# Performance work log

Hardware: AMD Instinct MI355X
Metric: run time of the kernel (lower is better)

## Reference

```python
import jax, jax.numpy as jnp
import numpy as np

EPS = 1e-5

def _ln(z, g, b):
    # LayerNorm over last axis (per the gammas/betas of shape (2, 3H))
    mu = jnp.mean(z, axis=-1, keepdims=True)
    var = jnp.var(z, axis=-1, keepdims=True)
    return g * (z - mu) * jax.lax.rsqrt(var + EPS) + b

def setup_inputs() -> dict:
    key = jax.random.key(0)
    ks = jax.random.split(key, 12)
    B, L, D_IN, H, A, DEPTH = 64, 512, 256, 256, 128, 4
    glorot = lambda k, sh: jax.random.normal(k, sh, jnp.float32) * np.sqrt(2.0 / (sh[0] + sh[1])).astype(np.float32)
    # variable-length prefix masks (bucketing/masking semantics of the layer)
    lengths = jax.random.randint(ks[0], (B, 1), L // 2, L + 1)
    mask = jnp.arange(L)[None, :] < lengths
    return {
        'x': jax.random.normal(ks[1], (B, L, D_IN), jnp.float32),
        'mask': mask,
        'W_emb': glorot(ks[2], (D_IN, H)),
        'b_emb': jnp.zeros((H,), jnp.float32),
        'W': glorot(ks[3], (H, 3 * H)),
        'U': glorot(ks[4], (H, 3 * H)),
        'b': jnp.zeros((3 * H,), jnp.float32),
        'W_action_1': glorot(ks[5], (H, A)),
        'U_action_1': glorot(ks[6], (H, A)),
        'b_action_1': jnp.zeros((A,), jnp.float32),
        'W_action_2': glorot(ks[7], (A, 2)),
        'b_action_2': jnp.zeros((2,), jnp.float32),
        'gammas': jnp.ones((2, 3 * H), jnp.float32),
        'betas': jnp.zeros((2, 3 * H), jnp.float32),
        'depth': DEPTH,
    }

def _run_depth(x_seq, m_seq, W, U, b, Wa1, Ua1, ba1, Wa2, ba2, gammas, betas):
    # x_seq: (L,B,H), m_seq: (L,B) bool
    H = W.shape[0]
    B = x_seq.shape[1]
    # precompute + layernorm the input projection for all steps (fusable)
    xp_all = _ln(jnp.einsum('lbh,hk->lbk', x_seq, W), gammas[0], betas[0])  # (L,B,3H)

    def step(h, inputs):
        xp, xt, mt = inputs  # (B,3H), (B,H), (B,)
        hp = _ln(h @ U, gammas[1], betas[1])
        r = jax.nn.sigmoid(xp[:, :H] + hp[:, :H] + b[:H])
        z = jax.nn.sigmoid(xp[:, H:2 * H] + hp[:, H:2 * H] + b[H:2 * H])
        hh = jnp.tanh(xp[:, 2 * H:] + r * hp[:, 2 * H:] + b[2 * H:])
        h_new = z * h + (1.0 - z) * hh
        # action-policy subnetwork (binary merge/propagate decision)
        logits = jnp.tanh(xt @ Wa1 + h @ Ua1 + ba1) @ Wa2 + ba2  # (B,2)
        pol = jax.nn.softmax(logits, axis=-1)
        act = (pol[:, 1] > pol[:, 0]) & mt
        h_out = jnp.where(mt[:, None], h_new, h)  # masked steps carry state
        return h_out, (h_out, act, pol)

    h0 = jnp.zeros((B, H), x_seq.dtype)
    _, (h_seq, act_seq, pol_seq) = jax.lax.scan(step, h0, (xp_all, x_seq, m_seq))
    return h_seq, act_seq, pol_seq

def reference(x, mask, W_emb, b_emb, W, U, b, W_action_1, U_action_1, b_action_1,
              W_action_2, b_action_2, gammas, betas, depth):
    # embedding projection, then time-major like the Theano scans
    h_seq = jnp.swapaxes(x @ W_emb + b_emb, 0, 1)  # (L,B,H)
    m_seq = jnp.swapaxes(mask, 0, 1)               # (L,B)
    actions, policies = [], []
    for _ in range(depth):  # vertical (tree-depth) scan: small fixed count
        h_new, act, pol = _run_depth(h_seq, m_seq, W, U, b,
                                     W_action_1, U_action_1, b_action_1,
                                     W_action_2, b_action_2, gammas, betas)
        actions.append(act)
        policies.append(pol)
        h_seq = h_new
        m_seq = m_seq & act  # tree collapse: only selected nodes survive upward
    output = h_seq[-1]  # (B,H) final hidden state of top layer
    action = jnp.stack(actions, 0).transpose(2, 0, 1)      # (B,depth,L)
    policy = jnp.stack(policies, 0).transpose(2, 0, 1, 3)  # (B,depth,L,2)
    return output, action, policy
```

## Files before the change

### kernel.cpp

```cpp
#include <hip/hip_runtime.h>
#include <hip/hip_bf16.h>
#include <math.h>

#define BB 64
#define LL 512
#define HH 256
#define H3 768
#define AA 128
#define NDEPTH 4
#define NROWS (LL*BB)

#define EXCH_U64_PER_CHAIN (2 * 3 * 256)

typedef float vf32x32 __attribute__((ext_vector_type(32)));

__global__ void maskcvt_kernel(const unsigned char* __restrict__ raw,
                               int* __restrict__ m)
{
    int i = blockIdx.x * blockDim.x + threadIdx.x;
    bool bytemode = (raw[1] == 1);
    int v;
    if (bytemode) v = raw[i] ? 1 : 0;
    else          v = (((const int*)raw)[i] != 0) ? 1 : 0;
    m[i] = v;
}

__global__ __launch_bounds__(512) void mkidx_kernel(
    const int* __restrict__ m,
    int* __restrict__ rowidx,
    int* __restrict__ nact)
{
    const int b    = blockIdx.x;
    const int tid  = threadIdx.x;
    const int lane = tid & 63;
    const int w    = tid >> 6;
    __shared__ int wcnt[8];
    int pred = m[b * LL + tid];
    unsigned long long bal = __ballot(pred != 0);
    int below = __popcll(bal & ((1ull << lane) - 1ull));
    if (lane == 63) wcnt[w] = __popcll(bal);
    __syncthreads();
    int woff = 0;
#pragma unroll
    for (int i = 0; i < 8; ++i) woff += (i < w) ? wcnt[i] : 0;
    if (pred) rowidx[b * LL + woff + below] = tid;
    if (tid == 511) nact[b] = woff + wcnt[7];
}

template<int MODE, int EPI>
__global__ __launch_bounds__(256) void gemm_kernel(
    const float* __restrict__ A, const float* __restrict__ Bm,
    const float* __restrict__ bias,
    float* __restrict__ C, int M, int N,
    const int* __restrict__ ridx, const int* __restrict__ nact)
{
    __shared__ float As[16][136];
    __shared__ float Bs[16][136];
    const int tid = threadIdx.x;
    const int tx = tid & 15, ty = tid >> 4;
    const int row0 = blockIdx.y * 128, col0 = blockIdx.x * 128;

    int arow0 = 0, arow1 = 0;
    if (MODE == 3) {
        const int bb = row0 >> 9;
        const int na = nact[bb];
        if ((row0 & 511) >= na) return;
        const int r0 = row0 + (tid >> 2);
        const int r1 = r0 + 64;
        const int l0 = ((r0 & 511) < na) ? ridx[r0] : 0;
        const int l1 = ((r1 & 511) < na) ? ridx[r1] : 0;
        arow0 = l0 * 64 + bb;
        arow1 = l1 * 64 + bb;
    }

    float acc[8][8];
#pragma unroll
    for (int i = 0; i < 8; ++i)
#pragma unroll
        for (int j = 0; j < 8; ++j) acc[i][j] = 0.f;

    for (int kk = 0; kk < 256; kk += 16) {
#pragma unroll
        for (int i = 0; i < 2; ++i) {
            int aid = i * 256 + tid;
            int r   = aid >> 2;
            int k4  = (aid & 3) << 2;
            int rr  = row0 + r;
            float4 v;
            if (MODE == 1) {
                v = *(const float4*)(A + (rr & 63) * 131072 + (rr >> 6) * 256 + kk + k4);
            } else {
                int ar = i ? arow1 : arow0;
                v = *(const float4*)(A + ar * 256 + kk + k4);
            }
            As[k4 + 0][r] = v.x; As[k4 + 1][r] = v.y;
            As[k4 + 2][r] = v.z; As[k4 + 3][r] = v.w;

            int bid = i * 256 + tid;
            int bk  = bid >> 5;
            int c4  = (bid & 31) << 2;
            float4 w = *(const float4*)(Bm + (kk + bk) * N + col0 + c4);
            *(float4*)&Bs[bk][c4] = w;
        }
        __syncthreads();
#pragma unroll
        for (int k = 0; k < 16; ++k) {
            float a[8], bb2[8];
            *(float4*)&a[0]   = *(const float4*)&As[k][ty * 8];
            *(float4*)&a[4]   = *(const float4*)&As[k][ty * 8 + 4];
            *(float4*)&bb2[0] = *(const float4*)&Bs[k][tx * 8];
            *(float4*)&bb2[4] = *(const float4*)&Bs[k][tx * 8 + 4];
#pragma unroll
            for (int i = 0; i < 8; ++i)
#pragma unroll
                for (int j = 0; j < 8; ++j)
                    acc[i][j] += a[i] * bb2[j];
        }
        __syncthreads();
    }

#pragma unroll
    for (int i = 0; i < 8; ++i) {
        int row  = row0 + ty * 8 + i;
        int colb = col0 + tx * 8;
        float vout[8];
#pragma unroll
        for (int j = 0; j < 8; ++j) {
            float v = acc[i][j];
            if (EPI == 1) v += bias[colb + j];
            vout[j] = v;
        }
        *(float4*)&C[row * N + colb]     = *(float4*)&vout[0];
        *(float4*)&C[row * N + colb + 4] = *(float4*)&vout[4];
    }
}

__global__ __launch_bounds__(256) void lnrows_kernel(
    float* __restrict__ XP, const float* __restrict__ g0,
    const float* __restrict__ b0, const float* __restrict__ gb,
    const int* __restrict__ nact)
{
    const int row = blockIdx.x;
    if ((row & 511) >= nact[row >> 9]) return;
    const int tid = threadIdx.x;
    float* p = XP + (long)row * H3;
    float v0 = p[tid], v1 = p[tid + 256], v2 = p[tid + 512];
    float s = v0 + v1 + v2;
    float q = v0 * v0 + v1 * v1 + v2 * v2;
#pragma unroll
    for (int off = 32; off >= 1; off >>= 1) {
        s += __shfl_xor(s, off);
        q += __shfl_xor(q, off);
    }
    __shared__ float rs4[4], rq4[4];
    if ((tid & 63) == 0) { rs4[tid >> 6] = s; rq4[tid >> 6] = q; }
    __syncthreads();
    float S = rs4[0] + rs4[1] + rs4[2] + rs4[3];
    float Q = rq4[0] + rq4[1] + rq4[2] + rq4[3];
    float mu  = S * (1.f / 768.f);
    float var = Q * (1.f / 768.f) - mu * mu;
    float r   = rsqrtf(var + 1e-5f);
    p[tid]       = g0[tid]       * (v0 - mu) * r + b0[tid]       + gb[tid];
    p[tid + 256] = g0[tid + 256] * (v1 - mu) * r + b0[tid + 256] + gb[tid + 256];
    p[tid + 512] = g0[tid + 512] * (v2 - mu) * r + b0[tid + 512] + gb[tid + 512];
}

__global__ __launch_bounds__(512, 2) void scan3_kernel(
    const float* __restrict__ XP,
    const float* __restrict__ U,
    const float* __restrict__ g1, const float* __restrict__ b1,
    const int* __restrict__ mask,
    float* __restrict__ Y,
    unsigned long long* __restrict__ exch,
    int seq0,
    const float* __restrict__ Xc,
    const float* __restrict__ Wa1,
    const float* __restrict__ ba1,
    float* __restrict__ XA)
{
    __shared__ float h_cur[256];
    __shared__ float part[16][256];
    __shared__ float xp_lds[768];
    __shared__ float g1s[768], b1s[768];
    __shared__ int   mk[512];
    __shared__ float reds[4], redq[4];
    __shared__ float As[16][136];
    __shared__ float Bs[16][136];

    const int tid = threadIdx.x;

    if (blockIdx.x >= 192) {
        const int t    = blockIdx.x - 192;
        const int row0 = t * 128;
        const int tx   = tid & 15;
        const int ty4  = tid >> 4;
        float xacc[4][8];
#pragma unroll
        for (int i = 0; i < 4; ++i)
#pragma unroll
            for (int j = 0; j < 8; ++j) xacc[i][j] = 0.f;

        for (int kk = 0; kk < 256; kk += 16) {
            {
                int r  = tid >> 2;
                int k4 = (tid & 3) << 2;
                float4 v = *(const float4*)(Xc + (row0 + r) * 256 + kk + k4);
                As[k4 + 0][r] = v.x; As[k4 + 1][r] = v.y;
                As[k4 + 2][r] = v.z; As[k4 + 3][r] = v.w;
            }
            {
                int bk = tid >> 5;
                int c4 = (tid & 31) << 2;
                float4 w = *(const float4*)(Wa1 + (kk + bk) * AA + c4);
                *(float4*)&Bs[bk][c4] = w;
            }
            __syncthreads();
#pragma unroll
            for (int k = 0; k < 16; ++k) {
                float a[4], bb2[8];
                *(float4*)&a[0]   = *(const float4*)&As[k][ty4 * 4];
                *(float4*)&bb2[0] = *(const float4*)&Bs[k][tx * 8];
                *(float4*)&bb2[4] = *(const float4*)&Bs[k][tx * 8 + 4];
#pragma unroll
                for (int i = 0; i < 4; ++i)
#pragma unroll
                    for (int j = 0; j < 8; ++j)
                        xacc[i][j] += a[i] * bb2[j];
            }
            __syncthreads();
        }
#pragma unroll
        for (int i = 0; i < 4; ++i) {
            int row  = row0 + ty4 * 4 + i;
            int colb = tx * 8;
            float vout[8];
#pragma unroll
            for (int j = 0; j < 8; ++j) vout[j] = xacc[i][j] + ba1[colb + j];
            *(float4*)&XA[row * AA + colb]     = *(float4*)&vout[0];
            *(float4*)&XA[row * AA + colb + 4] = *(float4*)&vout[4];
        }
        return;
    }

    const int i0   = blockIdx.x;
    const int xcd  = i0 & 7;
    const int slot = i0 >> 3;
    const int b    = xcd + 8 * (slot / 3);
    const int s    = slot % 3;
    const int kg   = tid >> 5;
    const int cg   = tid & 31;
    const int q1   = (s + 1 >= 3) ? s - 2 : s + 1;
    const int q2   = (s + 2 >= 3) ? s - 1 : s + 2;

    vf32x32 u0v, u1v, u2v, u3v;
    {
        const volatile float* Uv = U;
        const int colbase = s * 256 + cg;
#pragma unroll
        for (int i = 0; i < 16; ++i) {
#pragma unroll
            for (int j = 0; j < 8; ++j) {
                const int f = i * 8 + j;
                float val = Uv[(kg * 16 + i) * H3 + colbase + 32 * j];
                if      (f < 32) u0v[f]      = val;
                else if (f < 64) u1v[f - 32] = val;
                else if (f < 96) u2v[f - 64] = val;
                else             u3v[f - 96] = val;
            }
        }
    }
    if (tid < 256) h_cur[tid] = 0.f;
    for (int i = tid; i < 768; i += 512) { g1s[i] = g1[i]; b1s[i] = b1[i]; }
    mk[tid] = mask[b * LL + tid];
    __syncthreads();

    unsigned long long* exb = exch + b * EXCH_U64_PER_CHAIN;
    int seq = seq0;

    for (int l = 0; l < LL; ++l) {
        if (!mk[l]) {
            if (s == 0 && tid < 64) {
                float4 hv = *(const float4*)&h_cur[tid * 4];
                *(float4*)&Y[((long)l * BB + b) * HH + tid * 4] = hv;
            }
            continue;
        }
        seq++;
        const int par = seq & 1;
        const int cs  = seq - seq0 - 1;

        float4 xr4;
        if (tid < 192) xr4 = *(const float4*)(XP + ((long)(b * LL + cs)) * H3 + tid * 4);

        float acc[8] = {0.f, 0.f, 0.f, 0.f, 0.f, 0.f, 0.f, 0.f};
#pragma unroll
        for (int i = 0; i < 4; ++i) {
            float4 hv = *(const float4*)&h_cur[kg * 16 + i * 4];
#pragma unroll
            for (int e = 0; e < 4; ++e) {
                const float hh = (e == 0) ? hv.x : (e == 1) ? hv.y
                               : (e == 2) ? hv.z : hv.w;
                const int ik = i * 4 + e;
#pragma unroll
                for (int j = 0; j < 8; ++j) {
                    const int f = ik * 8 + j;
                    const float uu = (f < 32) ? u0v[f]
                                   : (f < 64) ? u1v[f - 32]
                                   : (f < 96) ? u2v[f - 64]
                                   :            u3v[f - 96];
                    acc[j] += uu * hh;
                }
            }
        }
#pragma unroll
        for (int j = 0; j < 8; ++j)
            part[kg][cg + 32 * j] = acc[j];
        __syncthreads();

        if (tid < 192) *(float4*)&xp_lds[tid * 4] = xr4;

        float pre = 0.f, v0 = 0.f, v1 = 0.f, v2 = 0.f;
        if (tid < 256) {
            pre = part[0][tid];
#pragma unroll
            for (int gg = 1; gg < 16; ++gg) pre += part[gg][tid];

            unsigned long long pk =
                ((unsigned long long)(unsigned)seq << 32) |
                (unsigned long long)__float_as_uint(pre);
            __hip_atomic_store(&exb[(par * 3 + s) * 256 + tid], pk,
                               __ATOMIC_RELAXED, __HIP_MEMORY_SCOPE_AGENT);

            unsigned long long x1 = 0, x2 = 0;
            bool d1 = false, d2 = false;
            int spins = 0;
            do {
                unsigned long long t1 =
                    __hip_atomic_load(&exb[(par * 3 + q1) * 256 + tid],
                                      __ATOMIC_RELAXED, __HIP_MEMORY_SCOPE_AGENT);
                unsigned long long t2 =
                    __hip_atomic_load(&exb[(par * 3 + q2) * 256 + tid],
                                      __ATOMIC_RELAXED, __HIP_MEMORY_SCOPE_AGENT);
                if (!d1 && (int)(t1 >> 32) == seq) { x1 = t1; d1 = true; }
                if (!d2 && (int)(t2 >> 32) == seq) { x2 = t2; d2 = true; }
                if (++spins > 8) __builtin_amdgcn_s_sleep(1);
            } while (!(d1 && d2));
            float w1 = __uint_as_float((unsigned)x1);
            float w2 = __uint_as_float((unsigned)x2);
            v0 = (s == 0) ? pre : ((q1 == 0) ? w1 : w2);
            v1 = (s == 1) ? pre : ((q1 == 1) ? w1 : w2);
            v2 = (s == 2) ? pre : ((q1 == 2) ? w1 : w2);

            float st = v0 + v1 + v2;
            float qt = v0 * v0 + v1 * v1 + v2 * v2;
#pragma unroll
            for (int off = 32; off >= 1; off >>= 1) {
                st += __shfl_xor(st, off);
                qt += __shfl_xor(qt, off);
            }
            if ((tid & 63) == 0) { reds[tid >> 6] = st; redq[tid >> 6] = qt; }
        }
        __syncthreads();

        if (tid < 256) {
            float S = reds[0] + reds[1] + reds[2] + reds[3];
            float Q = redq[0] + redq[1] + redq[2] + redq[3];
            float mu = S * (1.f / 768.f);
            float rs = rsqrtf(Q * (1.f / 768.f) - mu * mu + 1e-5f);
            float hp_r = g1s[tid]       * (v0 - mu) * rs + b1s[tid];
            float hp_z = g1s[256 + tid] * (v1 - mu) * rs + b1s[256 + tid];
            float hp_h = g1s[512 + tid] * (v2 - mu) * rs + b1s[512 + tid];
            float xr = xp_lds[tid], xz = xp_lds[256 + tid], xh = xp_lds[512 + tid];
            float r  = 1.f / (1.f + expf(-(xr + hp_r)));
            float z  = 1.f / (1.f + expf(-(xz + hp_z)));
            float hh = tanhf(xh + r * hp_h);
            float o  = z * h_cur[tid] + (1.f - z) * hh;
            h_cur[tid] = o;
            if (s == 0) Y[((long)l * BB + b) * HH + tid] = o;
        }
        __syncthreads();
    }
}

__global__ __launch_bounds__(256) void gemmact_kernel(
    const float* __restrict__ Yprev,
    const float* __restrict__ Ua1,
    const float* __restrict__ XA,
    const float* __restrict__ Wa2,
    const float* __restrict__ ba2,
    const int* __restrict__ mask_in, int* __restrict__ mask_out,
    float* __restrict__ act_out, float* __restrict__ pol_out, int d)
{
    __shared__ float As[16][136];
    __shared__ float Bs[16][136];
    const int tid = threadIdx.x;
    const int tx = tid & 15, ty = tid >> 4;
    const int row0 = blockIdx.y * 128;

    float acc[8][8];
#pragma unroll
    for (int i = 0; i < 8; ++i)
#pragma unroll
        for (int j = 0; j < 8; ++j) acc[i][j] = 0.f;

    for (int kk = 0; kk < 256; kk += 16) {
#pragma unroll
        for (int i = 0; i < 2; ++i) {
            int aid = i * 256 + tid;
            int r   = aid >> 2;
            int k4  = (aid & 3) << 2;
            int rr  = row0 + r;
            float4 v;
            if (rr < 64) v = make_float4(0.f, 0.f, 0.f, 0.f);
            else         v = *(const float4*)(Yprev + (rr - 64) * 256 + kk + k4);
            As[k4 + 0][r] = v.x; As[k4 + 1][r] = v.y;
            As[k4 + 2][r] = v.z; As[k4 + 3][r] = v.w;

            int bid = i * 256 + tid;
            int bk  = bid >> 5;
            int c4  = (bid & 31) << 2;
            float4 w = *(const float4*)(Ua1 + (kk + bk) * AA + c4);
            *(float4*)&Bs[bk][c4] = w;
        }
        __syncthreads();
#pragma unroll
        for (int k = 0; k < 16; ++k) {
            float a[8], bb2[8];
            *(float4*)&a[0]   = *(const float4*)&As[k][ty * 8];
            *(float4*)&a[4]   = *(const float4*)&As[k][ty * 8 + 4];
            *(float4*)&bb2[0] = *(const float4*)&Bs[k][tx * 8];
            *(float4*)&bb2[4] = *(const float4*)&Bs[k][tx * 8 + 4];
#pragma unroll
            for (int i = 0; i < 8; ++i)
#pragma unroll
                for (int j = 0; j < 8; ++j)
                    acc[i][j] += a[i] * bb2[j];
        }
        __syncthreads();
    }

    float p0[8], p1[8];
#pragma unroll
    for (int i = 0; i < 8; ++i) { p0[i] = 0.f; p1[i] = 0.f; }
#pragma unroll
    for (int i = 0; i < 8; ++i) {
        int row  = row0 + ty * 8 + i;
#pragma unroll
        for (int j = 0; j < 8; ++j) {
            int c   = tx * 8 + j;
            float v = tanhf(acc[i][j] + XA[row * AA + c]);
            p0[i] += v * Wa2[c * 2];
            p1[i] += v * Wa2[c * 2 + 1];
        }
    }
#pragma unroll
    for (int off = 1; off < 16; off <<= 1) {
#pragma unroll
        for (int i = 0; i < 8; ++i) {
            p0[i] += __shfl_xor(p0[i], off);
            p1[i] += __shfl_xor(p1[i], off);
        }
    }
    if (tx == 0) {
#pragma unroll
        for (int i = 0; i < 8; ++i) {
            int row = row0 + ty * 8 + i;
            int l   = row >> 6, bb = row & 63;
            float l0 = p0[i] + ba2[0];
            float l1 = p1[i] + ba2[1];
            float m  = fmaxf(l0, l1);
            float e0 = expf(l0 - m), e1 = expf(l1 - m);
            float inv = 1.f / (e0 + e1);
            float q0 = e0 * inv, q1v = e1 * inv;
            int mt = mask_in[bb * LL + l];
            int a  = (q1v > q0) && mt;
            act_out[bb * (NDEPTH * LL) + d * LL + l] = a ? 1.f : 0.f;
            pol_out[bb * (NDEPTH * LL * 2) + d * (LL * 2) + l * 2 + 0] = q0;
            pol_out[bb * (NDEPTH * LL * 2) + d * (LL * 2) + l * 2 + 1] = q1v;
            mask_out[bb * LL + l] = a;
        }
    }
}

__global__ void final_copy_kernel(const float* __restrict__ X, float* __restrict__ out)
{
    int i = blockIdx.x * blockDim.x + threadIdx.x;
    int bb = i >> 8, j = i & 255;
    out[i] = X[((long)(LL - 1) * BB + bb) * HH + j];
}

extern "C" void kernel_launch(void* const* d_in, const int* in_sizes, int n_in,
                              void* d_out, int out_size, void* d_ws, size_t ws_size,
                              hipStream_t stream)
{
    const float* x      = (const float*)d_in[0];
    const void*  mraw   = d_in[1];
    const float* W_emb  = (const float*)d_in[2];
    const float* b_emb  = (const float*)d_in[3];
    const float* W      = (const float*)d_in[4];
    const float* U      = (const float*)d_in[5];
    const float* bias3  = (const float*)d_in[6];
    const float* Wa1    = (const float*)d_in[7];
    const float* Ua1    = (const float*)d_in[8];
    const float* ba1    = (const float*)d_in[9];
    const float* Wa2    = (const float*)d_in[10];
    const float* ba2    = (const float*)d_in[11];
    const float* gammas = (const float*)d_in[12];
    const float* betas  = (const float*)d_in[13];

    float* out = (float*)d_out;
    char*  ws  = (char*)d_ws;

    float* XP = (float*)(ws);
    float* X  = (float*)(ws + 100663296UL);
    float* Y  = (float*)(ws + 134217728UL);
    float* XA = (float*)(ws + 167772160UL);
    int*   m0 = (int*)(ws + 184549376UL);
    int*   m1 = (int*)(ws + 184680448UL);
    unsigned long long* exch_d = (unsigned long long*)(ws + 184811520UL);

    float* act_out = out + BB * HH;
    float* pol_out = act_out + BB * NDEPTH * LL;

    maskcvt_kernel<<<dim3(NROWS / 256), dim3(256), 0, stream>>>(
        (const unsigned char*)mraw, m0);

    gemm_kernel<1, 1><<<dim3(2, 256), dim3(256), 0, stream>>>(
        x, W_emb, b_emb, X, NROWS, HH, nullptr, nullptr);

    float* Xc = X; float* Yc = Y;
    int* mc = m0; int* mn = m1;

    for (int d = 0; d < NDEPTH; ++d) {
        int* rowidx = (int*)Yc;
        int* nactp  = ((int*)Yc) + NROWS;

        mkidx_kernel<<<dim3(BB), dim3(512), 0, stream>>>(mc, rowidx, nactp);

        gemm_kernel<3, 0><<<dim3(6, 256), dim3(256), 0, stream>>>(
            Xc, W, nullptr, XP, NROWS, H3, rowidx, nactp);
        lnrows_kernel<<<dim3(NROWS), dim3(256), 0, stream>>>(
            XP, gammas, betas, bias3, nactp);

        scan3_kernel<<<dim3(448), dim3(512), 0, stream>>>(
            XP, U, gammas + H3, betas + H3, mc, Yc, exch_d, d << 10,
            Xc, Wa1, ba1, XA);

        gemmact_kernel<<<dim3(1, 256), dim3(256), 0, stream>>>(
            Yc, Ua1, XA, Wa2, ba2, mc, mn, act_out, pol_out, d);

        { float* tmp = Xc; Xc = Yc; Yc = tmp; }
        { int* tmp = mc; mc = mn; mn = tmp; }
    }

    final_copy_kernel<<<dim3(BB), dim3(256), 0, stream>>>(Xc, out);
}
```

Baseline: 3.295 ms.

## Fuse action-policy GEMM into scan kernel with per-timestep counters

Removes the separate gemmact kernel. The extra blocks in the scan kernel now compute both the Ua1 and Wa1 projections, the tanh, the Wa2 projection and the softmax/action outputs. The extra blocks wait on per-timestep atomic counters that the recurrent blocks bump after writing each h row, so policy work overlaps the sequential scan instead of running after it, and the XA intermediate buffer is dropped. The cost is spin-waiting blocks, relaxed atomic stores and loads on Y, and a memset per call.

```diff
diff --git a/kernel.cpp b/kernel.cpp
--- a/kernel.cpp
+++ b/kernel.cpp
@@ -165,7 +165,7 @@
     p[tid + 512] = g0[tid + 512] * (v2 - mu) * r + b0[tid + 512] + gb[tid + 512];
 }
 
-__global__ __launch_bounds__(512, 2) void scan3_kernel(
+__global__ __launch_bounds__(512, 2) void scanact_kernel(
     const float* __restrict__ XP,
     const float* __restrict__ U,
     const float* __restrict__ g1, const float* __restrict__ b1,
@@ -174,73 +174,137 @@
     unsigned long long* __restrict__ exch,
     int seq0,
     const float* __restrict__ Xc,
-    const float* __restrict__ Wa1,
-    const float* __restrict__ ba1,
-    float* __restrict__ XA)
-{
-    __shared__ float h_cur[256];
-    __shared__ float part[16][256];
-    __shared__ float xp_lds[768];
-    __shared__ float g1s[768], b1s[768];
-    __shared__ int   mk[512];
-    __shared__ float reds[4], redq[4];
-    __shared__ float As[16][136];
-    __shared__ float Bs[16][136];
-
+    const float* __restrict__ Wa1, const float* __restrict__ ba1,
+    const float* __restrict__ Ua1,
+    const float* __restrict__ Wa2, const float* __restrict__ ba2,
+    int* __restrict__ mask_out,
+    float* __restrict__ act_out, float* __restrict__ pol_out,
+    int d,
+    int* __restrict__ cnt)
+{
+    __shared__ __align__(16) char smem[34816];
     const int tid = threadIdx.x;
 
     if (blockIdx.x >= 192) {
+        float (*As1)[136] = (float(*)[136])(smem);
+        float (*As2)[136] = (float(*)[136])(smem + 8704);
+        float (*Bs1)[136] = (float(*)[136])(smem + 17408);
+        float (*Bs2)[136] = (float(*)[136])(smem + 26112);
         const int t    = blockIdx.x - 192;
         const int row0 = t * 128;
-        const int tx   = tid & 15;
-        const int ty4  = tid >> 4;
-        float xacc[4][8];
+
+        if (tid == 0) {
+            const int target = 64 * (d + 1);
+            int spins = 0;
+            while (__hip_atomic_load(&cnt[2 * t], __ATOMIC_ACQUIRE,
+                                     __HIP_MEMORY_SCOPE_AGENT) < target) {
+                if (++spins > 8) __builtin_amdgcn_s_sleep(8);
+            }
+        }
+        __syncthreads();
+
+        const int tx = tid & 15;
+        const int ty = tid >> 4;
+        float acc[4][8];
 #pragma unroll
         for (int i = 0; i < 4; ++i)
 #pragma unroll
-            for (int j = 0; j < 8; ++j) xacc[i][j] = 0.f;
+            for (int j = 0; j < 8; ++j) acc[i][j] = 0.f;
 
         for (int kk = 0; kk < 256; kk += 16) {
             {
                 int r  = tid >> 2;
                 int k4 = (tid & 3) << 2;
-                float4 v = *(const float4*)(Xc + (row0 + r) * 256 + kk + k4);
-                As[k4 + 0][r] = v.x; As[k4 + 1][r] = v.y;
-                As[k4 + 2][r] = v.z; As[k4 + 3][r] = v.w;
+                int rr = row0 + r;
+                float4 v1;
+                if (rr < 64) v1 = make_float4(0.f, 0.f, 0.f, 0.f);
+                else {
+                    const float* yp = Y + (rr - 64) * 256 + kk + k4;
+                    v1.x = __hip_atomic_load(yp + 0, __ATOMIC_RELAXED, __HIP_MEMORY_SCOPE_AGENT);
+                    v1.y = __hip_atomic_load(yp + 1, __ATOMIC_RELAXED, __HIP_MEMORY_SCOPE_AGENT);
+                    v1.z = __hip_atomic_load(yp + 2, __ATOMIC_RELAXED, __HIP_MEMORY_SCOPE_AGENT);
+                    v1.w = __hip_atomic_load(yp + 3, __ATOMIC_RELAXED, __HIP_MEMORY_SCOPE_AGENT);
+                }
+                As1[k4 + 0][r] = v1.x; As1[k4 + 1][r] = v1.y;
+                As1[k4 + 2][r] = v1.z; As1[k4 + 3][r] = v1.w;
+                float4 v2 = *(const float4*)(Xc + rr * 256 + kk + k4);
+                As2[k4 + 0][r] = v2.x; As2[k4 + 1][r] = v2.y;
+                As2[k4 + 2][r] = v2.z; As2[k4 + 3][r] = v2.w;
             }
             {
                 int bk = tid >> 5;
                 int c4 = (tid & 31) << 2;
-                float4 w = *(const float4*)(Wa1 + (kk + bk) * AA + c4);
-                *(float4*)&Bs[bk][c4] = w;
+                *(float4*)&Bs1[bk][c4] = *(const float4*)(Ua1 + (kk + bk) * AA + c4);
+                *(float4*)&Bs2[bk][c4] = *(const float4*)(Wa1 + (kk + bk) * AA + c4);
             }
             __syncthreads();
 #pragma unroll
             for (int k = 0; k < 16; ++k) {
-                float a[4], bb2[8];
-                *(float4*)&a[0]   = *(const float4*)&As[k][ty4 * 4];
-                *(float4*)&bb2[0] = *(const float4*)&Bs[k][tx * 8];
-                *(float4*)&bb2[4] = *(const float4*)&Bs[k][tx * 8 + 4];
+                float a1[4], a2[4], w1[8], w2[8];
+                *(float4*)&a1[0] = *(const float4*)&As1[k][ty * 4];
+                *(float4*)&a2[0] = *(const float4*)&As2[k][ty * 4];
+                *(float4*)&w1[0] = *(const float4*)&Bs1[k][tx * 8];
+                *(float4*)&w1[4] = *(const float4*)&Bs1[k][tx * 8 + 4];
+                *(float4*)&w2[0] = *(const float4*)&Bs2[k][tx * 8];
+                *(float4*)&w2[4] = *(const float4*)&Bs2[k][tx * 8 + 4];
 #pragma unroll
                 for (int i = 0; i < 4; ++i)
 #pragma unroll
                     for (int j = 0; j < 8; ++j)
-                        xacc[i][j] += a[i] * bb2[j];
+                        acc[i][j] += a1[i] * w1[j] + a2[i] * w2[j];
             }
             __syncthreads();
         }
-#pragma unroll
-        for (int i = 0; i < 4; ++i) {
-            int row  = row0 + ty4 * 4 + i;
-            int colb = tx * 8;
-            float vout[8];
-#pragma unroll
-            for (int j = 0; j < 8; ++j) vout[j] = xacc[i][j] + ba1[colb + j];
-            *(float4*)&XA[row * AA + colb]     = *(float4*)&vout[0];
-            *(float4*)&XA[row * AA + colb + 4] = *(float4*)&vout[4];
+
+        float p0[4], p1[4];
+#pragma unroll
+        for (int i = 0; i < 4; ++i) { p0[i] = 0.f; p1[i] = 0.f; }
+#pragma unroll
+        for (int i = 0; i < 4; ++i)
+#pragma unroll
+            for (int j = 0; j < 8; ++j) {
+                int c   = tx * 8 + j;
+                float v = tanhf(acc[i][j] + ba1[c]);
+                p0[i] += v * Wa2[c * 2];
+                p1[i] += v * Wa2[c * 2 + 1];
+            }
+#pragma unroll
+        for (int off = 1; off < 16; off <<= 1)
+#pragma unroll
+            for (int i = 0; i < 4; ++i) {
+                p0[i] += __shfl_xor(p0[i], off);
+                p1[i] += __shfl_xor(p1[i], off);
+            }
+        if (tx == 0) {
+#pragma unroll
+            for (int i = 0; i < 4; ++i) {
+                int row = row0 + ty * 4 + i;
+                int l   = row >> 6, bb = row & 63;
+                float l0 = p0[i] + ba2[0];
+                float l1 = p1[i] + ba2[1];
+                float m  = fmaxf(l0, l1);
+                float e0 = expf(l0 - m), e1 = expf(l1 - m);
+                float inv = 1.f / (e0 + e1);
+                float q0 = e0 * inv, q1v = e1 * inv;
+                int mt = mask[bb * LL + l];
+                int a  = (q1v > q0) && mt;
+                act_out[bb * (NDEPTH * LL) + d * LL + l] = a ? 1.f : 0.f;
+                pol_out[bb * (NDEPTH * LL * 2) + d * (LL * 2) + l * 2 + 0] = q0;
+                pol_out[bb * (NDEPTH * LL * 2) + d * (LL * 2) + l * 2 + 1] = q1v;
+                mask_out[bb * LL + l] = a;
+            }
         }
         return;
     }
+
+    float* h_cur        = (float*)smem;
+    float (*part)[256]  = (float(*)[256])(smem + 1024);
+    float* xp_lds       = (float*)(smem + 17408);
+    float* g1s          = (float*)(smem + 20480);
+    float* b1s          = (float*)(smem + 23552);
+    int*   mk           = (int*)(smem + 26624);
+    float* reds         = (float*)(smem + 28672);
+    float* redq         = (float*)(smem + 28688);
 
     const int i0   = blockIdx.x;
     const int xcd  = i0 & 7;
@@ -279,9 +343,17 @@
 
     for (int l = 0; l < LL; ++l) {
         if (!mk[l]) {
-            if (s == 0 && tid < 64) {
-                float4 hv = *(const float4*)&h_cur[tid * 4];
-                *(float4*)&Y[((long)l * BB + b) * HH + tid * 4] = hv;
+            if (s == 0) {
+                if (tid < 64) {
+                    float* yp = Y + ((long)l * BB + b) * HH + tid * 4;
+                    const float* hc = h_cur + tid * 4;
+                    __hip_atomic_store(yp + 0, hc[0], __ATOMIC_RELAXED, __HIP_MEMORY_SCOPE_AGENT);
+                    __hip_atomic_store(yp + 1, hc[1], __ATOMIC_RELAXED, __HIP_MEMORY_SCOPE_AGENT);
+                    __hip_atomic_store(yp + 2, hc[2], __ATOMIC_RELAXED, __HIP_MEMORY_SCOPE_AGENT);
+                    __hip_atomic_store(yp + 3, hc[3], __ATOMIC_RELAXED, __HIP_MEMORY_SCOPE_AGENT);
+                }
+                if (tid == 0)
+                    __hip_atomic_fetch_add(&cnt[l], 1, __ATOMIC_RELEASE, __HIP_MEMORY_SCOPE_AGENT);
             }
             continue;
         }
@@ -376,109 +448,14 @@
             float hh = tanhf(xh + r * hp_h);
             float o  = z * h_cur[tid] + (1.f - z) * hh;
             h_cur[tid] = o;
-            if (s == 0) Y[((long)l * BB + b) * HH + tid] = o;
+            if (s == 0)
+                __hip_atomic_store(&Y[((long)l * BB + b) * HH + tid], o,
+                                   __ATOMIC_RELAXED, __HIP_MEMORY_SCOPE_AGENT);
         }
         __syncthreads();
-    }
-}
-
-__global__ __launch_bounds__(256) void gemmact_kernel(
-    const float* __restrict__ Yprev,
-    const float* __restrict__ Ua1,
-    const float* __restrict__ XA,
-    const float* __restrict__ Wa2,
-    const float* __restrict__ ba2,
-    const int* __restrict__ mask_in, int* __restrict__ mask_out,
-    float* __restrict__ act_out, float* __restrict__ pol_out, int d)
-{
-    __shared__ float As[16][136];
-    __shared__ float Bs[16][136];
-    const int tid = threadIdx.x;
-    const int tx = tid & 15, ty = tid >> 4;
-    const int row0 = blockIdx.y * 128;
-
-    float acc[8][8];
-#pragma unroll
-    for (int i = 0; i < 8; ++i)
-#pragma unroll
-        for (int j = 0; j < 8; ++j) acc[i][j] = 0.f;
-
-    for (int kk = 0; kk < 256; kk += 16) {
-#pragma unroll
-        for (int i = 0; i < 2; ++i) {
-            int aid = i * 256 + tid;
-            int r   = aid >> 2;
-            int k4  = (aid & 3) << 2;
-            int rr  = row0 + r;
-            float4 v;
-            if (rr < 64) v = make_float4(0.f, 0.f, 0.f, 0.f);
-            else         v = *(const float4*)(Yprev + (rr - 64) * 256 + kk + k4);
-            As[k4 + 0][r] = v.x; As[k4 + 1][r] = v.y;
-            As[k4 + 2][r] = v.z; As[k4 + 3][r] = v.w;
-
-            int bid = i * 256 + tid;
-            int bk  = bid >> 5;
-            int c4  = (bid & 31) << 2;
-            float4 w = *(const float4*)(Ua1 + (kk + bk) * AA + c4);
-            *(float4*)&Bs[bk][c4] = w;
-        }
-        __syncthreads();
-#pragma unroll
-        for (int k = 0; k < 16; ++k) {
-            float a[8], bb2[8];
-            *(float4*)&a[0]   = *(const float4*)&As[k][ty * 8];
-            *(float4*)&a[4]   = *(const float4*)&As[k][ty * 8 + 4];
-            *(float4*)&bb2[0] = *(const float4*)&Bs[k][tx * 8];
-            *(float4*)&bb2[4] = *(const float4*)&Bs[k][tx * 8 + 4];
-#pragma unroll
-            for (int i = 0; i < 8; ++i)
-#pragma unroll
-                for (int j = 0; j < 8; ++j)
-                    acc[i][j] += a[i] * bb2[j];
-        }
-        __syncthreads();
-    }
-
-    float p0[8], p1[8];
-#pragma unroll
-    for (int i = 0; i < 8; ++i) { p0[i] = 0.f; p1[i] = 0.f; }
-#pragma unroll
-    for (int i = 0; i < 8; ++i) {
-        int row  = row0 + ty * 8 + i;
-#pragma unroll
-        for (int j = 0; j < 8; ++j) {
-            int c   = tx * 8 + j;
-            float v = tanhf(acc[i][j] + XA[row * AA + c]);
-            p0[i] += v * Wa2[c * 2];
-            p1[i] += v * Wa2[c * 2 + 1];
-        }
-    }
-#pragma unroll
-    for (int off = 1; off < 16; off <<= 1) {
-#pragma unroll
-        for (int i = 0; i < 8; ++i) {
-            p0[i] += __shfl_xor(p0[i], off);
-            p1[i] += __shfl_xor(p1[i], off);
-        }
-    }
-    if (tx == 0) {
-#pragma unroll
-        for (int i = 0; i < 8; ++i) {
-            int row = row0 + ty * 8 + i;
-            int l   = row >> 6, bb = row & 63;
-            float l0 = p0[i] + ba2[0];
-            float l1 = p1[i] + ba2[1];
-            float m  = fmaxf(l0, l1);
-            float e0 = expf(l0 - m), e1 = expf(l1 - m);
-            float inv = 1.f / (e0 + e1);
-            float q0 = e0 * inv, q1v = e1 * inv;
-            int mt = mask_in[bb * LL + l];
-            int a  = (q1v > q0) && mt;
-            act_out[bb * (NDEPTH * LL) + d * LL + l] = a ? 1.f : 0.f;
-            pol_out[bb * (NDEPTH * LL * 2) + d * (LL * 2) + l * 2 + 0] = q0;
-            pol_out[bb * (NDEPTH * LL * 2) + d * (LL * 2) + l * 2 + 1] = q1v;
-            mask_out[bb * LL + l] = a;
-        }
+        if (s == 0 && tid == 0)
+            __hip_atomic_fetch_add(&cnt[l], 1,
+                                   __ATOMIC_RELEASE, __HIP_MEMORY_SCOPE_AGENT);
     }
 }
 
@@ -514,13 +491,15 @@
     float* XP = (float*)(ws);
     float* X  = (float*)(ws + 100663296UL);
     float* Y  = (float*)(ws + 134217728UL);
-    float* XA = (float*)(ws + 167772160UL);
     int*   m0 = (int*)(ws + 184549376UL);
     int*   m1 = (int*)(ws + 184680448UL);
     unsigned long long* exch_d = (unsigned long long*)(ws + 184811520UL);
+    int*   cnt = (int*)(ws + 185597952UL);
 
     float* act_out = out + BB * HH;
     float* pol_out = act_out + BB * NDEPTH * LL;
+
+    hipMemsetAsync(cnt, 0, LL * sizeof(int), stream);
 
     maskcvt_kernel<<<dim3(NROWS / 256), dim3(256), 0, stream>>>(
         (const unsigned char*)mraw, m0);
@@ -542,12 +521,9 @@
         lnrows_kernel<<<dim3(NROWS), dim3(256), 0, stream>>>(
             XP, gammas, betas, bias3, nactp);
 
-        scan3_kernel<<<dim3(448), dim3(512), 0, stream>>>(
+        scanact_kernel<<<dim3(448), dim3(512), 0, stream>>>(
             XP, U, gammas + H3, betas + H3, mc, Yc, exch_d, d << 10,
-            Xc, Wa1, ba1, XA);
-
-        gemmact_kernel<<<dim3(1, 256), dim3(256), 0, stream>>>(
-            Yc, Ua1, XA, Wa2, ba2, mc, mn, act_out, pol_out, d);
+            Xc, Wa1, ba1, Ua1, Wa2, ba2, mn, act_out, pol_out, d, cnt);
 
         { float* tmp = Xc; Xc = Yc; Yc = tmp; }
         { int* tmp = mc; mc = mn; mn = tmp; }
```

Result: slower. 8.300 ms (+151.9%).
